# Performance work log

Measured on AMD Instinct MI355X. Metric: run time of the kernel, lower is better.

Reference implementation:

```python
import jax, jax.numpy as jnp
import numpy as np

B, N, H, BD, P = 16, 128, 128, 64, 256

def setup_inputs() -> dict:
    key = jax.random.key(0)
    ks = jax.random.split(key, 10)
    s = lambda fan_in: 1.0 / np.sqrt(fan_in)
    return {
        "hidden_states": jax.random.normal(ks[0], (B, N, H), dtype=jnp.float32),
        "positions": jax.random.normal(ks[1], (B, N, 2), dtype=jnp.float32),
        "W1": jax.random.uniform(ks[2], (2, BD), jnp.float32, -s(2), s(2)),
        "b1": jax.random.uniform(ks[3], (BD,), jnp.float32, -s(2), s(2)),
        "W2": jax.random.uniform(ks[4], (H + BD, P), jnp.float32, -s(H + BD), s(H + BD)),
        "b2": jax.random.uniform(ks[5], (P,), jnp.float32, -s(H + BD), s(H + BD)),
        "W3": jax.random.uniform(ks[6], (P, P), jnp.float32, -s(P), s(P)),
        "b3": jax.random.uniform(ks[7], (P,), jnp.float32, -s(P), s(P)),
        "Wout": jax.random.uniform(ks[8], (P, P), jnp.float32, -s(P), s(P)),
        "bout": jax.random.uniform(ks[9], (P,), jnp.float32, -s(P), s(P)),
    }

def reference(hidden_states, positions, W1, b1, W2, b2, W3, b3, Wout, bout):
    b, n, h = hidden_states.shape
    # rel[b,i,j] = pos[b,j] - pos[b,i]  -> [B,N,N,2]
    rel = positions[:, None, :, :] - positions[:, :, None, :]
    enc = jax.nn.relu(rel @ W1 + b1)                       # [B,N,N,BD]
    hid = jnp.broadcast_to(hidden_states[:, None, :, :], (b, n, n, h))
    x = jnp.concatenate([hid, enc], axis=-1)               # [B,N,N,H+BD]
    emb = jax.nn.relu(x @ W2 + b2) @ W3 + b3               # [B,N,N,P]
    # mask self (j == i) with -inf before max-pool over neighbors j
    self_mask = jnp.eye(n, dtype=bool)[None, :, :, None]
    emb = jnp.where(self_mask, -jnp.inf, emb)
    pooled = emb.max(axis=2)                               # [B,N,P]
    return pooled @ Wout + bout
```

## Files before the change

kernel.cpp:

```cpp
#include <hip/hip_runtime.h>
#include <hip/hip_fp16.h>

using f16x4 = __attribute__((ext_vector_type(4))) _Float16;
using f16x8 = __attribute__((ext_vector_type(8))) _Float16;
using f32x4 = __attribute__((ext_vector_type(4))) float;
using f32x16 = __attribute__((ext_vector_type(16))) float;
using u32x4 = __attribute__((ext_vector_type(4))) unsigned int;

__device__ __forceinline__ f16x8 ld_f16x8(const void* p) {
    return *reinterpret_cast<const f16x8*>(p);
}
__device__ __forceinline__ f16x8 ldnt_f16x8(const void* p) {
    return __builtin_nontemporal_load(reinterpret_cast<const f16x8*>(p));
}
__device__ __forceinline__ u32x4 ldnt_u4(const void* p) {
    return __builtin_nontemporal_load(reinterpret_cast<const u32x4*>(p));
}

__global__ void sp_prep(const float* __restrict__ W2, const float* __restrict__ W3,
                        const float* __restrict__ pos, const float* __restrict__ W1,
                        const float* __restrict__ b1, const float* __restrict__ hs,
                        const float* __restrict__ b2,
                        _Float16* __restrict__ W2bt, _Float16* __restrict__ W3s,
                        _Float16* __restrict__ T1h, _Float16* __restrict__ T1bh,
                        _Float16* __restrict__ hp16) {
    __shared__ float sh[8 * 128];
    const int tid = threadIdx.x;
    const int t = blockIdx.x * 256 + tid;
    if (t < 16384) {
        int p = t >> 6, k = t & 63;
        W2bt[t] = (_Float16)W2[(128 + k) * 256 + p];
    }
    {
        int kk = t >> 12, rem = t & 4095;
        int row = rem >> 4, inner = rem & 15;
        int slot = inner >> 3, e = inner & 7;
        int h = slot ^ ((row >> 2) & 1);
        int k = kk * 16 + (e & 3) + 8 * (e >> 2) + 4 * h;
        W3s[t] = (_Float16)W3[k * 256 + row];
    }
#pragma unroll
    for (int h = 0; h < 2; ++h) {
        int idx = t + h * 65536;
        int row = idx >> 6, k = idx & 63;
        float v = pos[row * 2] * W1[k] + pos[row * 2 + 1] * W1[64 + k];
        T1h[idx]  = (_Float16)v;
        T1bh[idx] = (_Float16)(v + b1[k]);
    }
    const int rb = blockIdx.x * 8;
    for (int q = tid; q < 1024; q += 256) sh[q] = hs[rb * 128 + q];
    __syncthreads();
    float acc[8];
    float bb = b2[tid];
#pragma unroll
    for (int r = 0; r < 8; ++r) acc[r] = bb;
    for (int k = 0; k < 128; ++k) {
        float w = W2[k * 256 + tid];
#pragma unroll
        for (int r = 0; r < 8; ++r) acc[r] += sh[r * 128 + k] * w;
    }
    int tt = tid >> 5, rem = tid & 31;
    int q = rem >> 3, hi = (rem >> 2) & 1, rr = tid & 3;
    int widx = tt * 32 + hi * 16 + q * 4 + rr;
#pragma unroll
    for (int r = 0; r < 8; ++r) hp16[(rb + r) * 256 + widx] = (_Float16)acc[r];
}

__global__ __launch_bounds__(256, 2) void sp_main(
    const float* __restrict__ b3,
    const _Float16* __restrict__ hp16, const _Float16* __restrict__ W2bt,
    const _Float16* __restrict__ W3s, const _Float16* __restrict__ T1h,
    const _Float16* __restrict__ T1bh, float* __restrict__ pool) {
    __shared__ __align__(16) char sW3[16][4096];
    __shared__ _Float16 sPoolH[4][8][128];

    const int bid = blockIdx.x;
    const int ig = bid & 15, ph = (bid >> 4) & 1, b = bid >> 5;
    const int tid = threadIdx.x;
    const int wj = tid >> 6, lane = tid & 63;
    const int l31 = lane & 31, hi = lane >> 5;

    {
        const u32x4* W3v = (const u32x4*)W3s;
        u32x4* dst = (u32x4*)sW3;
#pragma unroll
        for (int c = 0; c < 16; ++c)
            dst[c * 256 + tid] = ldnt_u4(W3v + c * 512 + ph * 256 + tid);
    }

    const int jl = wj * 32 + l31;
    const _Float16* tjb = T1bh + (b * 128 + jl) * 64 + hi * 8;
    const _Float16* tib = T1h + (b * 128) * 64 + hi * 8;
    const _Float16* hpb = hp16 + (b * 128 + jl) * 256;
    const int slotB = (hi ^ ((l31 >> 2) & 1)) * 16;

    __syncthreads();

#pragma unroll 1
    for (int ii2 = 0; ii2 < 4; ++ii2) {
        const int i0 = ig * 8 + ii2 * 2;
        const int i1 = i0 + 1;

        const _Float16* w2p = W2bt;
        const _Float16* hpp = hpb;
        asm volatile("" : "+v"(w2p), "+v"(hpp));

        f16x8 hpA_c = ldnt_f16x8(hpp + hi * 16);
        f16x8 hpB_c = ldnt_f16x8(hpp + hi * 16 + 8);

        f16x8 benc[2][4];
#pragma unroll
        for (int s = 0; s < 4; ++s) {
            f16x8 tbv = ldnt_f16x8(tjb + s * 16);
            f16x8 cv0 = ldnt_f16x8(tib + i0 * 64 + s * 16);
            f16x8 cv1 = ldnt_f16x8(tib + i1 * 64 + s * 16);
#pragma unroll
            for (int e = 0; e < 8; ++e) {
                _Float16 d0 = tbv[e] - cv0[e];
                _Float16 d1 = tbv[e] - cv1[e];
                benc[0][s][e] = d0 > (_Float16)0 ? d0 : (_Float16)0;
                benc[1][s][e] = d1 > (_Float16)0 ? d1 : (_Float16)0;
            }
        }

        f32x16 eacc[2][4];
#pragma unroll
        for (int iq = 0; iq < 2; ++iq)
#pragma unroll
            for (int nt = 0; nt < 4; ++nt)
#pragma unroll
                for (int r = 0; r < 16; ++r) eacc[iq][nt][r] = 0.f;

#pragma unroll
        for (int t = 0; t < 8; ++t) {
            f32x16 a0, a1;
#pragma unroll
            for (int r = 0; r < 16; ++r) { a0[r] = 0.f; a1[r] = 0.f; }
#pragma unroll
            for (int s = 0; s < 4; ++s) {
                f16x8 aw = ld_f16x8(w2p + (t * 32 + l31) * 64 + s * 16 + hi * 8);
                a0 = __builtin_amdgcn_mfma_f32_32x32x16_f16(aw, benc[0][s], a0, 0, 0, 0);
                a1 = __builtin_amdgcn_mfma_f32_32x32x16_f16(aw, benc[1][s], a1, 0, 0, 0);
            }
            f16x8 hpA_n = hpA_c, hpB_n = hpB_c;
            if (t < 7) {
                hpA_n = ldnt_f16x8(hpp + (t + 1) * 32 + hi * 16);
                hpB_n = ldnt_f16x8(hpp + (t + 1) * 32 + hi * 16 + 8);
            }
            f16x8 u00, u01, u10, u11;
#pragma unroll
            for (int e = 0; e < 4; ++e) {
                _Float16 v;
                v = (_Float16)a0[e]      + hpA_c[e];     u00[e]     = v > (_Float16)0 ? v : (_Float16)0;
                v = (_Float16)a0[e + 4]  + hpA_c[e + 4]; u00[e + 4] = v > (_Float16)0 ? v : (_Float16)0;
                v = (_Float16)a0[e + 8]  + hpB_c[e];     u01[e]     = v > (_Float16)0 ? v : (_Float16)0;
                v = (_Float16)a0[e + 12] + hpB_c[e + 4]; u01[e + 4] = v > (_Float16)0 ? v : (_Float16)0;
                v = (_Float16)a1[e]      + hpA_c[e];     u10[e]     = v > (_Float16)0 ? v : (_Float16)0;
                v = (_Float16)a1[e + 4]  + hpA_c[e + 4]; u10[e + 4] = v > (_Float16)0 ? v : (_Float16)0;
                v = (_Float16)a1[e + 8]  + hpB_c[e];     u11[e]     = v > (_Float16)0 ? v : (_Float16)0;
                v = (_Float16)a1[e + 12] + hpB_c[e + 4]; u11[e + 4] = v > (_Float16)0 ? v : (_Float16)0;
            }
#pragma unroll
            for (int nt = 0; nt < 4; ++nt) {
                const char* rowp = (const char*)sW3 + (nt * 32 + l31) * 32 + slotB;
                f16x8 bf0 = ld_f16x8(rowp + (2 * t) * 4096);
                f16x8 bf1 = ld_f16x8(rowp + (2 * t + 1) * 4096);
                eacc[0][nt] = __builtin_amdgcn_mfma_f32_32x32x16_f16(u00, bf0, eacc[0][nt], 0, 0, 0);
                eacc[1][nt] = __builtin_amdgcn_mfma_f32_32x32x16_f16(u10, bf0, eacc[1][nt], 0, 0, 0);
                eacc[0][nt] = __builtin_amdgcn_mfma_f32_32x32x16_f16(u01, bf1, eacc[0][nt], 0, 0, 0);
                eacc[1][nt] = __builtin_amdgcn_mfma_f32_32x32x16_f16(u11, bf1, eacc[1][nt], 0, 0, 0);
            }
            hpA_c = hpA_n;
            hpB_c = hpB_n;
        }

#pragma unroll
        for (int iq = 0; iq < 2; ++iq) {
            const int i = iq ? i1 : i0;
#pragma unroll
            for (int nt = 0; nt < 4; ++nt) {
                float m = -INFINITY;
#pragma unroll
                for (int r = 0; r < 16; ++r) {
                    int jrow = wj * 32 + (r & 3) + 8 * (r >> 2) + 4 * hi;
                    float v = eacc[iq][nt][r];
                    if (jrow != i) m = fmaxf(m, v);
                }
                m = fmaxf(m, __shfl_xor(m, 32));
                if (lane < 32) sPoolH[wj][ii2 * 2 + iq][nt * 32 + l31] = (_Float16)m;
            }
        }
    }
    __syncthreads();

#pragma unroll
    for (int q = 0; q < 4; ++q) {
        int idx = q * 256 + tid;
        int ii = idx >> 7, t = idx & 127;
        float v = fmaxf(fmaxf((float)sPoolH[0][ii][t], (float)sPoolH[1][ii][t]),
                        fmaxf((float)sPoolH[2][ii][t], (float)sPoolH[3][ii][t]));
        int p = ph * 128 + t;
        pool[(b * 128 + ig * 8 + ii) * 256 + p] = v + b3[p];
    }
}

__global__ void sp_out(const float* __restrict__ Wout, const float* __restrict__ bout,
                       float* __restrict__ io) {
    __shared__ float sp[4 * 256];
    int rb = blockIdx.x * 4;
    int tid = threadIdx.x;
    for (int t = tid; t < 1024; t += 256) sp[t] = io[rb * 256 + t];
    __syncthreads();
    float acc[4];
    float bb = bout[tid];
#pragma unroll
    for (int r = 0; r < 4; ++r) acc[r] = bb;
    for (int k = 0; k < 256; ++k) {
        float w = Wout[k * 256 + tid];
#pragma unroll
        for (int r = 0; r < 4; ++r) acc[r] += sp[r * 256 + k] * w;
    }
#pragma unroll
    for (int r = 0; r < 4; ++r) io[(rb + r) * 256 + tid] = acc[r];
}

extern "C" void kernel_launch(void* const* d_in, const int* in_sizes, int n_in,
                              void* d_out, int out_size, void* d_ws, size_t ws_size,
                              hipStream_t stream) {
    const float* hs   = (const float*)d_in[0];
    const float* pos  = (const float*)d_in[1];
    const float* W1   = (const float*)d_in[2];
    const float* b1   = (const float*)d_in[3];
    const float* W2   = (const float*)d_in[4];
    const float* b2   = (const float*)d_in[5];
    const float* W3   = (const float*)d_in[6];
    const float* b3   = (const float*)d_in[7];
    const float* Wout = (const float*)d_in[8];
    const float* bout = (const float*)d_in[9];
    float* out = (float*)d_out;

    _Float16* hp16 = (_Float16*)d_ws;
    _Float16* W2bt = (_Float16*)((char*)d_ws + (1 << 20));
    _Float16* W3s  = (_Float16*)((char*)d_ws + (1 << 20) + 32768);
    _Float16* T1h  = (_Float16*)((char*)d_ws + (1 << 20) + 32768 + 131072);
    _Float16* T1bh = (_Float16*)((char*)d_ws + (1 << 20) + 32768 + 131072 + 262144);

    sp_prep<<<256, 256, 0, stream>>>(W2, W3, pos, W1, b1, hs, b2,
                                     W2bt, W3s, T1h, T1bh, hp16);
    sp_main<<<512, 256, 0, stream>>>(b3, hp16, W2bt, W3s, T1h, T1bh, out);
    sp_out<<<512, 256, 0, stream>>>(Wout, bout, out);
}
```

Before: 83.54 us.

## Merge both P-halves into one 512-thread block and add MFMA setprio hints

Blocks that previously each handled half of the P outputs for the same (batch, i-group) are merged into a single 512-thread block. Eight waves now share one full copy of W3 in LDS (128KB) and the two halves are reduced together in the epilogue. The same i-group data no longer has to be loaded twice across separate blocks, but the larger LDS footprint may limit how many blocks fit on each CU. It also wraps the MFMA sections in s_setprio hints to favor matrix issue.

```diff
diff --git a/kernel.cpp b/kernel.cpp
--- a/kernel.cpp
+++ b/kernel.cpp
@@ -66,18 +66,20 @@
     for (int r = 0; r < 8; ++r) hp16[(rb + r) * 256 + widx] = (_Float16)acc[r];
 }
 
-__global__ __launch_bounds__(256, 2) void sp_main(
+__global__ __launch_bounds__(512, 2) void sp_main(
     const float* __restrict__ b3,
     const _Float16* __restrict__ hp16, const _Float16* __restrict__ W2bt,
     const _Float16* __restrict__ W3s, const _Float16* __restrict__ T1h,
     const _Float16* __restrict__ T1bh, float* __restrict__ pool) {
-    __shared__ __align__(16) char sW3[16][4096];
-    __shared__ _Float16 sPoolH[4][8][128];
+    __shared__ __align__(16) char sW3[16][8192];
+    __shared__ _Float16 sPoolH[8][8][128];
 
     const int bid = blockIdx.x;
-    const int ig = bid & 15, ph = (bid >> 4) & 1, b = bid >> 5;
+    const int ig = bid & 15, b = bid >> 4;
     const int tid = threadIdx.x;
-    const int wj = tid >> 6, lane = tid & 63;
+    const int wj8 = tid >> 6;
+    const int jw = wj8 & 3, ph = wj8 >> 2;
+    const int lane = tid & 63;
     const int l31 = lane & 31, hi = lane >> 5;
 
     {
@@ -85,14 +87,15 @@
         u32x4* dst = (u32x4*)sW3;
 #pragma unroll
         for (int c = 0; c < 16; ++c)
-            dst[c * 256 + tid] = ldnt_u4(W3v + c * 512 + ph * 256 + tid);
-    }
-
-    const int jl = wj * 32 + l31;
+            dst[c * 512 + tid] = ldnt_u4(W3v + c * 512 + tid);
+    }
+
+    const int jl = jw * 32 + l31;
     const _Float16* tjb = T1bh + (b * 128 + jl) * 64 + hi * 8;
     const _Float16* tib = T1h + (b * 128) * 64 + hi * 8;
     const _Float16* hpb = hp16 + (b * 128 + jl) * 256;
     const int slotB = (hi ^ ((l31 >> 2) & 1)) * 16;
+    const int phbase = ph * 4096;
 
     __syncthreads();
 
@@ -136,12 +139,14 @@
             f32x16 a0, a1;
 #pragma unroll
             for (int r = 0; r < 16; ++r) { a0[r] = 0.f; a1[r] = 0.f; }
+            __builtin_amdgcn_s_setprio(1);
 #pragma unroll
             for (int s = 0; s < 4; ++s) {
                 f16x8 aw = ld_f16x8(w2p + (t * 32 + l31) * 64 + s * 16 + hi * 8);
                 a0 = __builtin_amdgcn_mfma_f32_32x32x16_f16(aw, benc[0][s], a0, 0, 0, 0);
                 a1 = __builtin_amdgcn_mfma_f32_32x32x16_f16(aw, benc[1][s], a1, 0, 0, 0);
             }
+            __builtin_amdgcn_s_setprio(0);
             f16x8 hpA_n = hpA_c, hpB_n = hpB_c;
             if (t < 7) {
                 hpA_n = ldnt_f16x8(hpp + (t + 1) * 32 + hi * 16);
@@ -160,16 +165,18 @@
                 v = (_Float16)a1[e + 8]  + hpB_c[e];     u11[e]     = v > (_Float16)0 ? v : (_Float16)0;
                 v = (_Float16)a1[e + 12] + hpB_c[e + 4]; u11[e + 4] = v > (_Float16)0 ? v : (_Float16)0;
             }
+            __builtin_amdgcn_s_setprio(1);
 #pragma unroll
             for (int nt = 0; nt < 4; ++nt) {
-                const char* rowp = (const char*)sW3 + (nt * 32 + l31) * 32 + slotB;
-                f16x8 bf0 = ld_f16x8(rowp + (2 * t) * 4096);
-                f16x8 bf1 = ld_f16x8(rowp + (2 * t + 1) * 4096);
+                const char* rowp = (const char*)sW3 + phbase + (nt * 32 + l31) * 32 + slotB;
+                f16x8 bf0 = ld_f16x8(rowp + (2 * t) * 8192);
+                f16x8 bf1 = ld_f16x8(rowp + (2 * t + 1) * 8192);
                 eacc[0][nt] = __builtin_amdgcn_mfma_f32_32x32x16_f16(u00, bf0, eacc[0][nt], 0, 0, 0);
                 eacc[1][nt] = __builtin_amdgcn_mfma_f32_32x32x16_f16(u10, bf0, eacc[1][nt], 0, 0, 0);
                 eacc[0][nt] = __builtin_amdgcn_mfma_f32_32x32x16_f16(u01, bf1, eacc[0][nt], 0, 0, 0);
                 eacc[1][nt] = __builtin_amdgcn_mfma_f32_32x32x16_f16(u11, bf1, eacc[1][nt], 0, 0, 0);
             }
+            __builtin_amdgcn_s_setprio(0);
             hpA_c = hpA_n;
             hpB_c = hpB_n;
         }
@@ -182,12 +189,12 @@
                 float m = -INFINITY;
 #pragma unroll
                 for (int r = 0; r < 16; ++r) {
-                    int jrow = wj * 32 + (r & 3) + 8 * (r >> 2) + 4 * hi;
+                    int jrow = jw * 32 + (r & 3) + 8 * (r >> 2) + 4 * hi;
                     float v = eacc[iq][nt][r];
                     if (jrow != i) m = fmaxf(m, v);
                 }
                 m = fmaxf(m, __shfl_xor(m, 32));
-                if (lane < 32) sPoolH[wj][ii2 * 2 + iq][nt * 32 + l31] = (_Float16)m;
+                if (lane < 32) sPoolH[wj8][ii2 * 2 + iq][nt * 32 + l31] = (_Float16)m;
             }
         }
     }
@@ -195,11 +202,12 @@
 
 #pragma unroll
     for (int q = 0; q < 4; ++q) {
-        int idx = q * 256 + tid;
-        int ii = idx >> 7, t = idx & 127;
-        float v = fmaxf(fmaxf((float)sPoolH[0][ii][t], (float)sPoolH[1][ii][t]),
-                        fmaxf((float)sPoolH[2][ii][t], (float)sPoolH[3][ii][t]));
-        int p = ph * 128 + t;
+        int idx = q * 512 + tid;
+        int ii = idx >> 8, p = idx & 255;
+        int php = p >> 7, t = p & 127;
+        float v = fmaxf(
+            fmaxf((float)sPoolH[php * 4 + 0][ii][t], (float)sPoolH[php * 4 + 1][ii][t]),
+            fmaxf((float)sPoolH[php * 4 + 2][ii][t], (float)sPoolH[php * 4 + 3][ii][t]));
         pool[(b * 128 + ig * 8 + ii) * 256 + p] = v + b3[p];
     }
 }
@@ -247,6 +255,6 @@
 
     sp_prep<<<256, 256, 0, stream>>>(W2, W3, pos, W1, b1, hs, b2,
                                      W2bt, W3s, T1h, T1bh, hp16);
-    sp_main<<<512, 256, 0, stream>>>(b3, hp16, W2bt, W3s, T1h, T1bh, out);
+    sp_main<<<256, 512, 0, stream>>>(b3, hp16, W2bt, W3s, T1h, T1bh, out);
     sp_out<<<512, 256, 0, stream>>>(Wout, bout, out);
 }
```

Result: no change. 84.72 us (+1.4%).
